# Kernel optimization log

Measured on AMD Instinct MI355X. Metric: run time of the kernel, lower is better.

Reference implementation:

```python
import jax, jax.numpy as jnp
import numpy as np

B, N, D = 8, 128, 512

def setup_inputs() -> dict:
    key = jax.random.key(0)
    ks = jax.random.split(key, 8)
    def lin_w(k, fan_in, shape):
        bound = 1.0 / np.sqrt(fan_in)
        return jax.random.uniform(k, shape, jnp.float32, -bound, bound)
    return {
        "features": jax.random.normal(ks[0], (B, N, D), jnp.float32),
        "positions": jax.random.uniform(ks[1], (B, N, 2), jnp.float32),
        "W1": lin_w(ks[2], 2 * D + 2, (2 * D + 2, D)),
        "b1": lin_w(ks[3], 2 * D + 2, (D,)),
        "W2": lin_w(ks[4], D, (D, D // 2)),
        "b2": lin_w(ks[5], D, (D // 2,)),
        "W3": lin_w(ks[6], D // 2, (D // 2, 4)),
        "b3": lin_w(ks[7], D // 2, (4,)),
    }

def reference(features, positions, W1, b1, W2, b2, W3, b3):
    d = features.shape[-1]
    # Split first linear: concat([f1, f2, pos_diff]) @ W1 == f1@W1a + f2@W1b + pos_diff@W1c
    W1a, W1b, W1c = W1[:d], W1[d:2 * d], W1[2 * d:]
    h1 = jnp.einsum("bnd,dk->bnk", features, W1a)          # broadcast over axis 2 (j)
    h2 = jnp.einsum("bmd,dk->bmk", features, W1b)          # broadcast over axis 1 (i)
    pos_diff = positions[:, :, None, :] - positions[:, None, :, :]  # [B,N,N,2]
    h = h1[:, :, None, :] + h2[:, None, :, :] + jnp.einsum("bnmp,pk->bnmk", pos_diff, W1c) + b1
    h = jax.nn.relu(h)
    h = jax.nn.relu(jnp.einsum("bnmk,kl->bnml", h, W2) + b2)
    return jnp.einsum("bnml,lo->bnmo", h, W3) + b3          # [B,N,N,4]
```

## Files before the change

kernel.cpp:

```cpp
#include <hip/hip_runtime.h>
#include <hip/hip_bf16.h>

typedef unsigned short u16;
typedef unsigned int u32;
typedef __attribute__((ext_vector_type(8))) short bf16x8;
typedef __attribute__((ext_vector_type(4))) float floatx4;

__device__ __forceinline__ float bflo(u32 u){ union{u32 i; float f;}v; v.i=u<<16; return v.f; }
__device__ __forceinline__ float bfhi(u32 u){ union{u32 i; float f;}v; v.i=u&0xFFFF0000u; return v.f; }
__device__ __forceinline__ u16 f2bf(float f){
    union{float f;u32 i;}v; v.f=f; u32 r=v.i+0x7FFFu+((v.i>>16)&1u); return (u16)(r>>16);
}
__device__ __forceinline__ u32 pkbf(float a, float b){
    union { __hip_bfloat162 h; u32 u; } cv;
    cv.h = __float22bfloat162_rn(float2{a, b});
    return cv.u;
}

#define DD 512
#define NTOK 128

__global__ __launch_bounds__(512) void prep_k(
    const float* __restrict__ features, const float* __restrict__ W1,
    const float* __restrict__ W2, const float* __restrict__ b1,
    u16* __restrict__ Hf1b, u16* __restrict__ Hf2, u16* __restrict__ W2T)
{
    const int z = blockIdx.z;
    const int tid = threadIdx.x;

    if (z == 2) {
        __shared__ u16 tile[32][33];
        const int tx = tid & 31, ty = tid >> 5;
        const int r0 = blockIdx.x * 32, c0 = blockIdx.y * 32;
#pragma unroll
        for (int i = 0; i < 2; ++i) {
            int r = ty + i * 16;
            tile[r][tx] = f2bf(W2[(size_t)(r0 + r) * 256 + (c0 + tx)]);
        }
        __syncthreads();
#pragma unroll
        for (int i = 0; i < 2; ++i) {
            int c = ty + i * 16;
            W2T[(size_t)(c0 + c) * 512 + (r0 + tx)] = tile[tx][c];
        }
        return;
    }

    const int bM = blockIdx.x, bN = blockIdx.y;
    u16* outp = z ? Hf2 : Hf1b;
    __shared__ __align__(16) u16 At[64 * 64];
    __shared__ __align__(16) u16 Btl[64 * 64];
    const int wid = tid >> 6, lane = tid & 63, lrow = lane & 15, quad = lane >> 4;
    const int wm = wid >> 1, wn = wid & 1;

    floatx4 acc[2];
    acc[0] = (floatx4)(0.0f); acc[1] = (floatx4)(0.0f);

    const int m = tid >> 3, seg = tid & 7, sw = m & 7;
    const int kr = tid >> 3, csB = tid & 7;

    for (int kc = 0; kc < 8; ++kc) {
        const int k0 = kc * 64;
        {
            const float4* src = (const float4*)(features + (size_t)(bM * 64 + m) * DD + k0 + seg * 8);
            float4 f0 = src[0], f1 = src[1];
            *(uint4*)(At + m * 64 + ((seg ^ sw) << 3)) =
                make_uint4(pkbf(f0.x, f0.y), pkbf(f0.z, f0.w), pkbf(f1.x, f1.y), pkbf(f1.z, f1.w));
        }
        {
            const float4* src = (const float4*)(W1 + (size_t)(z * 512 + k0 + kr) * DD + bN * 64 + csB * 8);
            float4 g0 = src[0], g1 = src[1];
            float f[8] = { g0.x, g0.y, g0.z, g0.w, g1.x, g1.y, g1.z, g1.w };
            const int chunkB = (kr >> 3), offB = kr & 7;
#pragma unroll
            for (int i = 0; i < 8; ++i) {
                int c = csB * 8 + i;
                Btl[c * 64 + ((chunkB ^ i) << 3) + offB] = f2bf(f[i]);
            }
        }
        __syncthreads();
#pragma unroll
        for (int ks = 0; ks < 2; ++ks) {
            const int ch = ks * 4 + quad;
            int r = wm * 16 + lrow;
            bf16x8 afr = *(const bf16x8*)(At + r * 64 + ((ch ^ (r & 7)) << 3));
#pragma unroll
            for (int j = 0; j < 2; ++j) {
                int c = wn * 32 + j * 16 + lrow;
                bf16x8 bfr = *(const bf16x8*)(Btl + c * 64 + ((ch ^ (c & 7)) << 3));
                acc[j] = __builtin_amdgcn_mfma_f32_16x16x32_bf16(afr, bfr, acc[j], 0, 0, 0);
            }
        }
        __syncthreads();
    }
#pragma unroll
    for (int j = 0; j < 2; ++j) {
        int col = bN * 64 + wn * 32 + j * 16 + lrow;
        float bb = z ? 0.0f : b1[col];
#pragma unroll
        for (int r = 0; r < 4; ++r) {
            int row = bM * 64 + wm * 16 + quad * 4 + r;
            outp[(size_t)row * DD + col] = f2bf(acc[j][r] + bb);
        }
    }
}

__global__ __launch_bounds__(512) void fused_main(
    const u16* __restrict__ Hf1b, const u16* __restrict__ Hf2,
    const u16* __restrict__ W2T, const float* __restrict__ W1,
    const float* __restrict__ b2, const float* __restrict__ W3,
    const float* __restrict__ b3, const float* __restrict__ positions,
    float* __restrict__ out)
{
    const int b = blockIdx.x, n = blockIdx.y;
    const int tid = threadIdx.x;
    const int base_bn = b * NTOK + n;
    const int wid = tid >> 6, lane = tid & 63, lrow = lane & 15, quad = lane >> 4;

    __shared__ __align__(16) u16 c0b[DD], c1b[DD], s1b[DD];
    __shared__ __align__(16) char mbuf[49152];
    u16* Atile = (u16*)mbuf;
    u16* Btile = (u16*)(mbuf + 16384);
    u16* gh    = (u16*)mbuf;
    u16* w3t   = (u16*)(mbuf + 34816);

    {
        int k = tid;
        c0b[k] = f2bf(W1[(size_t)1024 * DD + k]);
        c1b[k] = f2bf(W1[(size_t)1025 * DD + k]);
        s1b[k] = Hf1b[(size_t)base_bn * DD + k];
    }
    const int mrow = tid >> 2, seg = tid & 3, swA = mrow & 7;
    float px, py;
    {
        float pnx = positions[(size_t)base_bn * 2 + 0];
        float pny = positions[(size_t)base_bn * 2 + 1];
        px = pnx - positions[(size_t)(b * NTOK + mrow) * 2 + 0];
        py = pny - positions[(size_t)(b * NTOK + mrow) * 2 + 1];
    }
    const int csrc = lane >> 3, wsrc = lane & 7;
    const u16* bsrc_lane = W2T + csrc * DD + ((wsrc ^ csrc) << 3);
    __syncthreads();

    const int wm = wid >> 2, wn = wid & 3;
    floatx4 acc[4][4];
#pragma unroll
    for (int i = 0; i < 4; ++i)
#pragma unroll
        for (int j = 0; j < 4; ++j) acc[i][j] = (floatx4)(0.0f);

    const u16* hf2p = Hf2 + (size_t)(b * NTOK + mrow) * DD;

    for (int kc = 0; kc < 8; ++kc) {
        const int k0 = kc * 64;
#pragma unroll
        for (int q = 0; q < 4; ++q) {
            const int slot = wid * 4 + q;
            __builtin_amdgcn_global_load_lds(
                (const __attribute__((address_space(1))) u32*)(bsrc_lane + slot * 8 * DD + k0),
                (__attribute__((address_space(3))) u32*)(Btile + slot * 512), 16, 0, 0);
        }

        const int kb = k0 + seg * 16;
        {
            uint4 hv = *(const uint4*)(hf2p + kb);
            uint4 hw = *(const uint4*)(hf2p + kb + 8);
            uint4 sv = *(const uint4*)(s1b + kb);
            uint4 sw2 = *(const uint4*)(s1b + kb + 8);
            uint4 av = *(const uint4*)(c0b + kb);
            uint4 aw = *(const uint4*)(c0b + kb + 8);
            uint4 bv = *(const uint4*)(c1b + kb);
            uint4 bw = *(const uint4*)(c1b + kb + 8);
            auto hp = [&](u32 h, u32 s, u32 ca, u32 cb) -> u32 {
                float h0 = bflo(h) + bflo(s) + px * bflo(ca) + py * bflo(cb);
                float h1 = bfhi(h) + bfhi(s) + px * bfhi(ca) + py * bfhi(cb);
                return pkbf(fmaxf(h0, 0.0f), fmaxf(h1, 0.0f));
            };
            uint4 o0 = make_uint4(hp(hv.x, sv.x, av.x, bv.x), hp(hv.y, sv.y, av.y, bv.y),
                                  hp(hv.z, sv.z, av.z, bv.z), hp(hv.w, sv.w, av.w, bv.w));
            uint4 o1 = make_uint4(hp(hw.x, sw2.x, aw.x, bw.x), hp(hw.y, sw2.y, aw.y, bw.y),
                                  hp(hw.z, sw2.z, aw.z, bw.z), hp(hw.w, sw2.w, aw.w, bw.w));
            *(uint4*)(Atile + mrow * 64 + (((seg * 2    ) ^ swA) << 3)) = o0;
            *(uint4*)(Atile + mrow * 64 + (((seg * 2 + 1) ^ swA) << 3)) = o1;
        }
        __syncthreads();
#pragma unroll
        for (int ks = 0; ks < 2; ++ks) {
            const int ch = ks * 4 + quad;
            bf16x8 afr[4], bfr[4];
#pragma unroll
            for (int i = 0; i < 4; ++i) {
                int r = wm * 64 + i * 16 + lrow;
                afr[i] = *(const bf16x8*)(Atile + r * 64 + ((ch ^ (r & 7)) << 3));
            }
#pragma unroll
            for (int j = 0; j < 4; ++j) {
                int c = wn * 64 + j * 16 + lrow;
                bfr[j] = *(const bf16x8*)(Btile + c * 64 + ((ch ^ (c & 7)) << 3));
            }
#pragma unroll
            for (int i = 0; i < 4; ++i)
#pragma unroll
                for (int j = 0; j < 4; ++j)
                    acc[i][j] = __builtin_amdgcn_mfma_f32_16x16x32_bf16(afr[i], bfr[j], acc[i][j], 0, 0, 0);
        }
        __syncthreads();
    }

    {
        int c = tid & 15, kb2 = tid >> 4;
        int k0w = kb2 * 8;
        u32 wv[4];
#pragma unroll
        for (int p = 0; p < 4; ++p) {
            int ka = k0w + p * 2;
            u16 va = (c < 4) ? f2bf(W3[ka * 4 + c])       : (u16)0;
            u16 vb = (c < 4) ? f2bf(W3[(ka + 1) * 4 + c]) : (u16)0;
            wv[p] = (u32)va | ((u32)vb << 16);
        }
        *(uint2*)(w3t + c * 264 + k0w)     = make_uint2(wv[0], wv[1]);
        *(uint2*)(w3t + c * 264 + k0w + 4) = make_uint2(wv[2], wv[3]);
    }

    float b2v[4];
#pragma unroll
    for (int j = 0; j < 4; ++j) b2v[j] = b2[wn * 64 + j * 16 + lrow];

    const int smrow = wid * 16;
    floatx4 acc3 = (floatx4)(0.0f);
#pragma unroll
    for (int half = 0; half < 2; ++half) {
        __syncthreads();
        if ((wn >> 1) == half) {
#pragma unroll
            for (int i = 0; i < 4; ++i)
#pragma unroll
                for (int j = 0; j < 4; ++j)
#pragma unroll
                    for (int r = 0; r < 4; ++r) {
                        int row = wm * 64 + i * 16 + quad * 4 + r;
                        int col = (wn & 1) * 64 + j * 16 + lrow;
                        gh[row * 136 + col] = f2bf(fmaxf(acc[i][j][r] + b2v[j], 0.0f));
                    }
        }
        __syncthreads();
#pragma unroll
        for (int ks = 0; ks < 4; ++ks) {
            bf16x8 gfrag = *(const bf16x8*)(gh + (smrow + lrow) * 136 + ks * 32 + quad * 8);
            bf16x8 wfrag = *(const bf16x8*)(w3t + lrow * 264 + half * 128 + ks * 32 + quad * 8);
            acc3 = __builtin_amdgcn_mfma_f32_16x16x32_bf16(gfrag, wfrag, acc3, 0, 0, 0);
        }
    }
    if (lrow < 4) {
        float bo = b3[lrow];
#pragma unroll
        for (int r = 0; r < 4; ++r) {
            int row = smrow + quad * 4 + r;
            out[(size_t)base_bn * 512 + row * 4 + lrow] = acc3[r] + bo;
        }
    }
}

extern "C" void kernel_launch(void* const* d_in, const int* in_sizes, int n_in,
                              void* d_out, int out_size, void* d_ws, size_t ws_size,
                              hipStream_t stream)
{
    const float* features  = (const float*)d_in[0];
    const float* positions = (const float*)d_in[1];
    const float* W1 = (const float*)d_in[2];
    const float* b1 = (const float*)d_in[3];
    const float* W2 = (const float*)d_in[4];
    const float* b2 = (const float*)d_in[5];
    const float* W3 = (const float*)d_in[6];
    const float* b3 = (const float*)d_in[7];
    float* out = (float*)d_out;

    char* ws = (char*)d_ws;
    u16* W2T  = (u16*)(ws);
    u16* Hf1b = (u16*)(ws + 262144);
    u16* Hf2  = (u16*)(ws + 1310720);

    prep_k<<<dim3(16, 8, 3), 512, 0, stream>>>(features, W1, W2, b1, Hf1b, Hf2, W2T);
    fused_main<<<dim3(8, 128), 512, 0, stream>>>(Hf1b, Hf2, W2T, W1, b2, W3, b3,
                                                 positions, out);
}
```

Measured before the change: 128.7 us.

## Double-buffer K-loop tiles with 32-wide chunks to overlap loads and MFMA

Splits the GEMM K-loop into 16 chunks of 32 and double-buffers the A and B LDS tiles, so the W2T global-to-LDS load and the relu-prologue A computation for the next chunk run before the MFMAs on the current chunk. It also prefetches the Hf2 register loads one step ahead, uses a new 4-way XOR swizzle for the 32-wide rows, and needs only one barrier per iteration. The intent is to hide global load latency and cut barrier stalls. The cost is more iterations with less MFMA work each, and a full vmcnt(0) wait every iteration that may limit how much overlap is achieved.

```diff
diff --git a/kernel.cpp b/kernel.cpp
--- a/kernel.cpp
+++ b/kernel.cpp
@@ -119,10 +119,10 @@
 
     __shared__ __align__(16) u16 c0b[DD], c1b[DD], s1b[DD];
     __shared__ __align__(16) char mbuf[49152];
-    u16* Atile = (u16*)mbuf;
-    u16* Btile = (u16*)(mbuf + 16384);
-    u16* gh    = (u16*)mbuf;
-    u16* w3t   = (u16*)(mbuf + 34816);
+    u16* Ab  = (u16*)mbuf;
+    u16* Bb  = (u16*)(mbuf + 16384);
+    u16* gh  = (u16*)mbuf;
+    u16* w3t = (u16*)(mbuf + 34816);
 
     {
         int k = tid;
@@ -130,7 +130,8 @@
         c1b[k] = f2bf(W1[(size_t)1025 * DD + k]);
         s1b[k] = Hf1b[(size_t)base_bn * DD + k];
     }
-    const int mrow = tid >> 2, seg = tid & 3, swA = mrow & 7;
+    const int mrow = tid >> 2, seg = tid & 3;
+    const int awoff = mrow * 32 + ((seg ^ ((mrow >> 2) & 3)) << 3);
     float px, py;
     {
         float pnx = positions[(size_t)base_bn * 2 + 0];
@@ -138,8 +139,9 @@
         px = pnx - positions[(size_t)(b * NTOK + mrow) * 2 + 0];
         py = pny - positions[(size_t)(b * NTOK + mrow) * 2 + 1];
     }
-    const int csrc = lane >> 3, wsrc = lane & 7;
-    const u16* bsrc_lane = W2T + csrc * DD + ((wsrc ^ csrc) << 3);
+    const u32 wsw = (lane & 3) ^ ((lane >> 4) & 3);
+    const u16* bsrc_lane = W2T + (size_t)(wid * 32 + (lane >> 2)) * DD + (wsw << 3);
+    const int permR = ((quad ^ ((lrow >> 2) & 3)) << 3);
     __syncthreads();
 
     const int wm = wid >> 2, wn = wid & 3;
@@ -151,60 +153,63 @@
 
     const u16* hf2p = Hf2 + (size_t)(b * NTOK + mrow) * DD;
 
-    for (int kc = 0; kc < 8; ++kc) {
-        const int k0 = kc * 64;
-#pragma unroll
-        for (int q = 0; q < 4; ++q) {
-            const int slot = wid * 4 + q;
+    auto hp = [&](u32 h, u32 s, u32 ca, u32 cb) -> u32 {
+        float h0 = bflo(h) + bflo(s) + px * bflo(ca) + py * bflo(cb);
+        float h1 = bfhi(h) + bfhi(s) + px * bfhi(ca) + py * bfhi(cb);
+        return pkbf(fmaxf(h0, 0.0f), fmaxf(h1, 0.0f));
+    };
+    auto STAGE = [&](int tn, int bs) {
+#pragma unroll
+        for (int q = 0; q < 2; ++q) {
             __builtin_amdgcn_global_load_lds(
-                (const __attribute__((address_space(1))) u32*)(bsrc_lane + slot * 8 * DD + k0),
-                (__attribute__((address_space(3))) u32*)(Btile + slot * 512), 16, 0, 0);
-        }
-
-        const int kb = k0 + seg * 16;
+                (const __attribute__((address_space(1))) u32*)(bsrc_lane + q * 8192 + tn * 32),
+                (__attribute__((address_space(3))) u32*)(Bb + bs * 8192 + (wid * 2 + q) * 512),
+                16, 0, 0);
+        }
+    };
+    auto ACOMP = [&](int tn, int bs, uint4 hv) {
+        const int kb = tn * 32 + seg * 8;
+        uint4 sv = *(const uint4*)(s1b + kb);
+        uint4 av = *(const uint4*)(c0b + kb);
+        uint4 bv = *(const uint4*)(c1b + kb);
+        *(uint4*)(Ab + bs * 4096 + awoff) = make_uint4(
+            hp(hv.x, sv.x, av.x, bv.x), hp(hv.y, sv.y, av.y, bv.y),
+            hp(hv.z, sv.z, av.z, bv.z), hp(hv.w, sv.w, av.w, bv.w));
+    };
+
+    uint4 hcur = *(const uint4*)(hf2p + seg * 8);
+    STAGE(0, 0);
+    ACOMP(0, 0, hcur);
+    hcur = *(const uint4*)(hf2p + 32 + seg * 8);
+    asm volatile("s_waitcnt vmcnt(0) lgkmcnt(0)" ::: "memory");
+    __builtin_amdgcn_s_barrier();
+
+#pragma unroll
+    for (int t = 0; t < 16; ++t) {
+        const int p = t & 1;
+        if (t < 15) {
+            STAGE(t + 1, p ^ 1);
+            uint4 hnext = hcur;
+            if (t < 14) hnext = *(const uint4*)(hf2p + (t + 2) * 32 + seg * 8);
+            ACOMP(t + 1, p ^ 1, hcur);
+            hcur = hnext;
+        }
         {
-            uint4 hv = *(const uint4*)(hf2p + kb);
-            uint4 hw = *(const uint4*)(hf2p + kb + 8);
-            uint4 sv = *(const uint4*)(s1b + kb);
-            uint4 sw2 = *(const uint4*)(s1b + kb + 8);
-            uint4 av = *(const uint4*)(c0b + kb);
-            uint4 aw = *(const uint4*)(c0b + kb + 8);
-            uint4 bv = *(const uint4*)(c1b + kb);
-            uint4 bw = *(const uint4*)(c1b + kb + 8);
-            auto hp = [&](u32 h, u32 s, u32 ca, u32 cb) -> u32 {
-                float h0 = bflo(h) + bflo(s) + px * bflo(ca) + py * bflo(cb);
-                float h1 = bfhi(h) + bfhi(s) + px * bfhi(ca) + py * bfhi(cb);
-                return pkbf(fmaxf(h0, 0.0f), fmaxf(h1, 0.0f));
-            };
-            uint4 o0 = make_uint4(hp(hv.x, sv.x, av.x, bv.x), hp(hv.y, sv.y, av.y, bv.y),
-                                  hp(hv.z, sv.z, av.z, bv.z), hp(hv.w, sv.w, av.w, bv.w));
-            uint4 o1 = make_uint4(hp(hw.x, sw2.x, aw.x, bw.x), hp(hw.y, sw2.y, aw.y, bw.y),
-                                  hp(hw.z, sw2.z, aw.z, bw.z), hp(hw.w, sw2.w, aw.w, bw.w));
-            *(uint4*)(Atile + mrow * 64 + (((seg * 2    ) ^ swA) << 3)) = o0;
-            *(uint4*)(Atile + mrow * 64 + (((seg * 2 + 1) ^ swA) << 3)) = o1;
-        }
-        __syncthreads();
-#pragma unroll
-        for (int ks = 0; ks < 2; ++ks) {
-            const int ch = ks * 4 + quad;
             bf16x8 afr[4], bfr[4];
 #pragma unroll
-            for (int i = 0; i < 4; ++i) {
-                int r = wm * 64 + i * 16 + lrow;
-                afr[i] = *(const bf16x8*)(Atile + r * 64 + ((ch ^ (r & 7)) << 3));
-            }
-#pragma unroll
-            for (int j = 0; j < 4; ++j) {
-                int c = wn * 64 + j * 16 + lrow;
-                bfr[j] = *(const bf16x8*)(Btile + c * 64 + ((ch ^ (c & 7)) << 3));
-            }
+            for (int i = 0; i < 4; ++i)
+                afr[i] = *(const bf16x8*)(Ab + p * 4096 + (wm * 64 + i * 16 + lrow) * 32 + permR);
+#pragma unroll
+            for (int j = 0; j < 4; ++j)
+                bfr[j] = *(const bf16x8*)(Bb + p * 8192 + (wn * 64 + j * 16 + lrow) * 32 + permR);
 #pragma unroll
             for (int i = 0; i < 4; ++i)
 #pragma unroll
                 for (int j = 0; j < 4; ++j)
                     acc[i][j] = __builtin_amdgcn_mfma_f32_16x16x32_bf16(afr[i], bfr[j], acc[i][j], 0, 0, 0);
         }
-        __syncthreads();
+        asm volatile("s_waitcnt vmcnt(0) lgkmcnt(0)" ::: "memory");
+        __builtin_amdgcn_s_barrier();
     }
 
     {
```

After: 130.7 us. Within noise of the previous version (+1.6%).
